# Kernel tuning notes

Hardware: AMD Instinct MI355X
Metric: run time of the kernel (lower is better)

The kernel has to match this reference:

```python
import jax, jax.numpy as jnp
import numpy as np

N_NODES = 100000


def gcn_conv(x, W, src, dst, n):
    """PyG GCNConv with bias=False: add self-loops, symmetric norm, scatter-add."""
    h = x @ W  # [N, out]
    # degree including self-loop (all edge weights = 1)
    deg = jnp.zeros((n,), dtype=x.dtype).at[dst].add(1.0) + 1.0
    inv_sqrt = jax.lax.rsqrt(deg)  # deg >= 1 so safe
    edge_norm = inv_sqrt[src] * inv_sqrt[dst]  # [E]
    # neighbor aggregation: out_i = sum_{j->i} norm_ji * h_j
    agg = jnp.zeros_like(h).at[dst].add(h[src] * edge_norm[:, None])
    # self-loop contribution: norm_ii = 1/deg_i
    return agg + h * (inv_sqrt * inv_sqrt)[:, None]


def setup_inputs() -> dict:
    key = jax.random.key(0)
    k1, k2, k3, k4 = jax.random.split(key, 4)
    x = jax.random.normal(k1, (N_NODES, 128), dtype=jnp.float32)
    edge_index = jax.random.randint(k2, (2, 1600000), 0, N_NODES, dtype=jnp.int32)
    W1 = jax.random.normal(k3, (128, 64), dtype=jnp.float32) * (1.0 / np.sqrt(128))
    W2 = jax.random.normal(k4, (64, 40), dtype=jnp.float32) * (1.0 / np.sqrt(64))
    return {"x": x, "edge_index": edge_index, "W1": W1, "W2": W2}


def reference(x, edge_index, W1, W2):
    n = x.shape[0]
    src, dst = edge_index[0], edge_index[1]
    # layer 1 (dropout p=0.0 is identity) + relu
    h = jax.nn.relu(gcn_conv(x, W1, src, dst, n))
    # layer 2 + relu, then squeeze
    out = jax.nn.relu(gcn_conv(h, W2, src, dst, n))
    return jnp.squeeze(out)
```

## Files before the change

kernel.cpp:

```cpp
#include <hip/hip_runtime.h>
#include <hip/hip_fp16.h>


#define F0 128
#define F1 64
#define F2 40
#define SCAN_B 512
#define GEMM_BLKS 768
#define NRANK (GEMM_BLKS / 3)

__global__ void k_zero(int* __restrict__ cnt, int n) {
    const int i = blockIdx.x * blockDim.x + threadIdx.x;
    if (i < n) cnt[i] = 0;
}

__global__ __launch_bounds__(256) void k_gemmrank(const float* __restrict__ x,
                                                  const float* __restrict__ W,
                                                  __half* __restrict__ h,
                                                  const int* __restrict__ ei,
                                                  int* __restrict__ cnt,
                                                  int* __restrict__ rank,
                                                  int n, int E) {
    __shared__ float Wl[F0 * F1];
    __shared__ float xs[32 * F0];
    const int bid = blockIdx.x;
    const int tid = threadIdx.x;

    if ((bid % 3) == 2) {
        const int rb = bid / 3;
        const int stride = NRANK * 256;
#pragma unroll 4
        for (int e = rb * 256 + tid; e < E; e += stride)
            rank[e] = atomicAdd(&cnt[ei[E + e]], 1);
        return;
    }

    const int gid = bid - bid / 3;
    const int c = tid & 63;
    const int rq = tid >> 6;

    {
        float4* Wl4 = (float4*)Wl;
        const float4* Wg4 = (const float4*)W;
#pragma unroll
        for (int j = 0; j < (F0 * F1 / 4) / 256; ++j)
            Wl4[j * 256 + tid] = Wg4[j * 256 + tid];
    }
    __syncthreads();

    const int NG = GEMM_BLKS - NRANK;
    const int ntiles = (n + 31) >> 5;
    for (int tile = gid; tile < ntiles; tile += NG) {
        float4* xs4w = (float4*)xs;
#pragma unroll
        for (int j = 0; j < 4; ++j) {
            int fi = j * 256 + tid;
            int row = fi >> 5;
            int rg = tile * 32 + row;
            if (rg > n - 1) rg = n - 1;
            const float4* xrow = (const float4*)(x + (long long)rg * F0);
            xs4w[fi] = xrow[fi & 31];
        }
        __syncthreads();

        float acc[8] = {0.f,0.f,0.f,0.f,0.f,0.f,0.f,0.f};
#pragma unroll 2
        for (int b = 0; b < 32; ++b) {
            const float w0 = Wl[(4 * b + 0) * F1 + c];
            const float w1 = Wl[(4 * b + 1) * F1 + c];
            const float w2 = Wl[(4 * b + 2) * F1 + c];
            const float w3 = Wl[(4 * b + 3) * F1 + c];
#pragma unroll
            for (int i = 0; i < 8; ++i) {
                float4 xv = ((const float4*)xs)[(rq * 8 + i) * 32 + b];
                acc[i] = fmaf(xv.w, w3, fmaf(xv.z, w2, fmaf(xv.y, w1, fmaf(xv.x, w0, acc[i]))));
            }
        }

#pragma unroll
        for (int i = 0; i < 8; ++i) {
            int rg = tile * 32 + rq * 8 + i;
            if (rg < n) h[(long long)rg * F1 + c] = __float2half(acc[i]);
        }
        __syncthreads();
    }
}

__global__ __launch_bounds__(SCAN_B) void k_rsqrt_bsum(const int* __restrict__ cnt,
                                                       float* __restrict__ invs,
                                                       int* __restrict__ bsum, int n) {
    __shared__ int s[SCAN_B];
    const int t = threadIdx.x;
    const int i = blockIdx.x * SCAN_B + t;
    int c = 0;
    if (i < n) {
        c = cnt[i];
        invs[i] = rsqrtf((float)(c + 1));
    }
    s[t] = c;
    __syncthreads();
    for (int off = SCAN_B / 2; off > 0; off >>= 1) {
        if (t < off) s[t] += s[t + off];
        __syncthreads();
    }
    if (t == 0) bsum[blockIdx.x] = s[0];
}

__global__ __launch_bounds__(1024) void k_bscan(int* __restrict__ bsum, int nb) {
    __shared__ int s[1024];
    const int t = threadIdx.x;
    const int orig = (t < nb) ? bsum[t] : 0;
    s[t] = orig;
    __syncthreads();
    for (int off = 1; off < 1024; off <<= 1) {
        int add = (t >= off) ? s[t - off] : 0;
        __syncthreads();
        s[t] += add;
        __syncthreads();
    }
    if (t < nb) bsum[t] = s[t] - orig;
}

__global__ __launch_bounds__(SCAN_B) void k_scan3(const int* __restrict__ cnt,
                                                  const int* __restrict__ bsum,
                                                  int* __restrict__ rowptr, int n) {
    __shared__ int s[SCAN_B];
    const int t = threadIdx.x;
    const int i = blockIdx.x * SCAN_B + t;
    const int orig = (i < n) ? cnt[i] : 0;
    s[t] = orig;
    __syncthreads();
    for (int off = 1; off < SCAN_B; off <<= 1) {
        int add = (t >= off) ? s[t - off] : 0;
        __syncthreads();
        s[t] += add;
        __syncthreads();
    }
    const int excl = s[t] - orig + bsum[blockIdx.x];
    if (i < n) rowptr[i] = excl;
    if (i == n - 1) rowptr[n] = excl + orig;
}

__global__ void k_fill_scale(const int* __restrict__ ei, const int* __restrict__ rank,
                             const int* __restrict__ rowptr, int* __restrict__ csr4,
                             __half* __restrict__ h, const float* __restrict__ invs,
                             int E, int n, int gFILL) {
    const int bid = blockIdx.x;
    const int tid = threadIdx.x;
    if (bid < gFILL) {
        int e = bid * 1024 + tid;
#pragma unroll
        for (int j = 0; j < 4; ++j, e += 256) {
            if (e < E) {
                const int s = ei[e];
                const int d = ei[E + e];
                csr4[rowptr[d] + rank[e]] = s;
            }
        }
    } else {
        const int fb = bid - gFILL;
        const long long total4 = (long long)n * F1 / 4;
        long long i4 = (long long)fb * 256 + tid;
        const long long stride = (long long)2048 * 256;
        for (; i4 < total4; i4 += stride) {
            const int r = (int)(i4 >> 4);
            const float iv = invs[r];
            __half2* hp = (__half2*)h + i4 * 2;
            __half2 a = hp[0], b = hp[1];
            float2 af = __half22float2(a), bf = __half22float2(b);
            af.x *= iv; af.y *= iv; bf.x *= iv; bf.y *= iv;
            hp[0] = __float22half2_rn(af);
            hp[1] = __float22half2_rn(bf);
        }
    }
}

__global__ __launch_bounds__(256) void k_gemm2(const float* __restrict__ x,
                                               const float* __restrict__ W,
                                               const float* __restrict__ invs,
                                               __half* __restrict__ h, int n) {
    __shared__ float Wl[F1 * F2];
    __shared__ float xs[32 * F1];
    const int tid = threadIdx.x;
    const int c = tid & 63;
    const int rq = tid >> 6;

    for (int i = tid; i < F1 * F2; i += 256) Wl[i] = W[i];
    __syncthreads();

    const int ntiles = (n + 31) >> 5;
    for (int tile = blockIdx.x; tile < ntiles; tile += gridDim.x) {
        float4* xs4w = (float4*)xs;
#pragma unroll
        for (int j = 0; j < 2; ++j) {
            int fi = j * 256 + tid;
            int row = fi >> 4;
            int rg = tile * 32 + row;
            if (rg > n - 1) rg = n - 1;
            const float4* xrow = (const float4*)(x + (long long)rg * F1);
            xs4w[fi] = xrow[fi & 15];
        }
        __syncthreads();

        if (c < F2) {
            float acc[8] = {0.f,0.f,0.f,0.f,0.f,0.f,0.f,0.f};
#pragma unroll 2
            for (int b = 0; b < 16; ++b) {
                const float w0 = Wl[(4 * b + 0) * F2 + c];
                const float w1 = Wl[(4 * b + 1) * F2 + c];
                const float w2 = Wl[(4 * b + 2) * F2 + c];
                const float w3 = Wl[(4 * b + 3) * F2 + c];
#pragma unroll
                for (int i = 0; i < 8; ++i) {
                    float4 xv = ((const float4*)xs)[(rq * 8 + i) * 16 + b];
                    acc[i] = fmaf(xv.w, w3, fmaf(xv.z, w2, fmaf(xv.y, w1, fmaf(xv.x, w0, acc[i]))));
                }
            }
#pragma unroll
            for (int i = 0; i < 8; ++i) {
                int rg = tile * 32 + rq * 8 + i;
                if (rg < n) h[(long long)rg * F2 + c] = __float2half(acc[i] * invs[rg]);
            }
        }
        __syncthreads();
    }
}

__global__ __launch_bounds__(256) void k_gather64(const int* __restrict__ rowptr,
                                                  const int* __restrict__ csr4,
                                                  const float* __restrict__ invs,
                                                  const __half* __restrict__ h,
                                                  float* __restrict__ g, int n) {
    const int w = (blockIdx.x * blockDim.x + threadIdx.x) >> 6;
    const int lane = threadIdx.x & 63;
    if (w >= n) return;
    const int beg = rowptr[w];
    const int end = rowptr[w + 1];
    float acc0 = 0.f, acc1 = 0.f, acc2 = 0.f, acc3 = 0.f;
    int k = beg;
    for (; k + 8 <= end; k += 8) {
        const int s0 = csr4[k+0], s1 = csr4[k+1], s2 = csr4[k+2], s3 = csr4[k+3];
        const int s4 = csr4[k+4], s5 = csr4[k+5], s6 = csr4[k+6], s7 = csr4[k+7];
        const float v0 = __half2float(h[(long long)s0 * F1 + lane]);
        const float v1 = __half2float(h[(long long)s1 * F1 + lane]);
        const float v2 = __half2float(h[(long long)s2 * F1 + lane]);
        const float v3 = __half2float(h[(long long)s3 * F1 + lane]);
        const float v4 = __half2float(h[(long long)s4 * F1 + lane]);
        const float v5 = __half2float(h[(long long)s5 * F1 + lane]);
        const float v6 = __half2float(h[(long long)s6 * F1 + lane]);
        const float v7 = __half2float(h[(long long)s7 * F1 + lane]);
        acc0 += v0 + v4; acc1 += v1 + v5; acc2 += v2 + v6; acc3 += v3 + v7;
    }
    for (; k + 2 <= end; k += 2) {
        const int s0 = csr4[k], s1 = csr4[k+1];
        acc0 += __half2float(h[(long long)s0 * F1 + lane]);
        acc1 += __half2float(h[(long long)s1 * F1 + lane]);
    }
    if (k < end) {
        const int s0 = csr4[k];
        acc0 += __half2float(h[(long long)s0 * F1 + lane]);
    }
    const float iv = invs[w];
    const float self = __half2float(h[(long long)w * F1 + lane]);
    g[(long long)w * F1 + lane] = fmaxf(iv * (((acc0 + acc1) + (acc2 + acc3)) + self), 0.f);
}

__global__ __launch_bounds__(256) void k_gather40(const int* __restrict__ rowptr,
                                                  const int* __restrict__ csr4,
                                                  const float* __restrict__ invs,
                                                  const __half* __restrict__ h,
                                                  float* __restrict__ g, int n) {
    const int w = (blockIdx.x * blockDim.x + threadIdx.x) >> 6;
    const int lane = threadIdx.x & 63;
    if (w >= n) return;
    const int beg = rowptr[w];
    const int end = rowptr[w + 1];
    float acc0 = 0.f, acc1 = 0.f, acc2 = 0.f, acc3 = 0.f;
    int k = beg;
    if (lane < F2) {
        for (; k + 8 <= end; k += 8) {
            const int s0 = csr4[k+0], s1 = csr4[k+1], s2 = csr4[k+2], s3 = csr4[k+3];
            const int s4 = csr4[k+4], s5 = csr4[k+5], s6 = csr4[k+6], s7 = csr4[k+7];
            const float v0 = __half2float(h[(long long)s0 * F2 + lane]);
            const float v1 = __half2float(h[(long long)s1 * F2 + lane]);
            const float v2 = __half2float(h[(long long)s2 * F2 + lane]);
            const float v3 = __half2float(h[(long long)s3 * F2 + lane]);
            const float v4 = __half2float(h[(long long)s4 * F2 + lane]);
            const float v5 = __half2float(h[(long long)s5 * F2 + lane]);
            const float v6 = __half2float(h[(long long)s6 * F2 + lane]);
            const float v7 = __half2float(h[(long long)s7 * F2 + lane]);
            acc0 += v0 + v4; acc1 += v1 + v5; acc2 += v2 + v6; acc3 += v3 + v7;
        }
        for (; k + 2 <= end; k += 2) {
            const int s0 = csr4[k], s1 = csr4[k+1];
            acc0 += __half2float(h[(long long)s0 * F2 + lane]);
            acc1 += __half2float(h[(long long)s1 * F2 + lane]);
        }
        if (k < end) {
            const int s0 = csr4[k];
            acc0 += __half2float(h[(long long)s0 * F2 + lane]);
        }
        const float iv = invs[w];
        const float self = __half2float(h[(long long)w * F2 + lane]);
        g[(long long)w * F2 + lane] = fmaxf(iv * (((acc0 + acc1) + (acc2 + acc3)) + self), 0.f);
    }
}

extern "C" void kernel_launch(void* const* d_in, const int* in_sizes, int n_in,
                              void* d_out, int out_size, void* d_ws, size_t ws_size,
                              hipStream_t stream) {
    const float* x  = (const float*)d_in[0];
    const int*   ei = (const int*)d_in[1];
    const float* W1 = (const float*)d_in[2];
    const float* W2 = (const float*)d_in[3];
    float* out = (float*)d_out;
    const int n = in_sizes[0] / F0;
    const int E = in_sizes[1] / 2;

    const size_t np = ((size_t)n + 65) & ~(size_t)63;
    char* wsb = (char*)d_ws;
    int*    cnt    = (int*)wsb;
    int*    rowptr = cnt + np;
    float*  invs   = (float*)(rowptr + np);
    int*    rank   = (int*)(invs + np);
    int*    csr4   = rank + E;
    __half* h1h    = (__half*)(csr4 + E);
    float*  g1     = (float*)(h1h + (size_t)n * F1);
    int*    bsum   = (int*)(g1 + (size_t)n * F1);
    __half* h2h    = h1h;

    const int nb = (n + SCAN_B - 1) / SCAN_B;
    const int gN = (n + 255) / 256;
    const int gW = (int)(((long long)n * 64 + 255) / 256);
    const int gFILL = (E + 1023) / 1024;
    const int gFS = gFILL + 2048;

    hipLaunchKernelGGL(k_zero,      dim3(gN), dim3(256), 0, stream, cnt, n);
    hipLaunchKernelGGL(k_gemmrank,  dim3(GEMM_BLKS), dim3(256), 0, stream,
                       x, W1, h1h, ei, cnt, rank, n, E);
    hipLaunchKernelGGL(k_rsqrt_bsum, dim3(nb), dim3(SCAN_B), 0, stream, cnt, invs, bsum, n);
    hipLaunchKernelGGL(k_bscan,      dim3(1),  dim3(1024), 0, stream, bsum, nb);
    hipLaunchKernelGGL(k_scan3,      dim3(nb), dim3(SCAN_B), 0, stream, cnt, bsum, rowptr, n);
    hipLaunchKernelGGL(k_fill_scale, dim3(gFS), dim3(256), 0, stream,
                       ei, rank, rowptr, csr4, h1h, invs, E, n, gFILL);

    hipLaunchKernelGGL(k_gather64, dim3(gW), dim3(256), 0, stream, rowptr, csr4, invs, h1h, g1, n);
    hipLaunchKernelGGL(k_gemm2,    dim3(GEMM_BLKS), dim3(256), 0, stream, g1, W2, invs, h2h, n);
    hipLaunchKernelGGL(k_gather40, dim3(gW), dim3(256), 0, stream, rowptr, csr4, invs, h2h, out, n);
}
```

Baseline: 249.3 us.

## Split node range in halves and overlap fill, gather64 and gemm2 across stages

The CSR fill is split by destination-node half: the first half is filled alongside the h1 scaling, then a fused stage kernel fills the second half while gathering layer 1 for the first half. A second stage runs gemm2 on the first half while gathering the second half, and a final gemm2 covers the remaining half. h2 gets its own buffer instead of aliasing h1. The goal is to overlap independent work inside fused launches and keep the GPU busier, at the cost of each fill block reading the edge list twice and an extra launch.

```diff
diff --git a/kernel.cpp b/kernel.cpp
--- a/kernel.cpp
+++ b/kernel.cpp
@@ -8,6 +8,7 @@
 #define SCAN_B 512
 #define GEMM_BLKS 768
 #define NRANK (GEMM_BLKS / 3)
+#define STG_GM 512
 
 __global__ void k_zero(int* __restrict__ cnt, int n) {
     const int i = blockIdx.x * blockDim.x + threadIdx.x;
@@ -141,55 +142,42 @@
     if (i == n - 1) rowptr[n] = excl + orig;
 }
 
-__global__ void k_fill_scale(const int* __restrict__ ei, const int* __restrict__ rank,
-                             const int* __restrict__ rowptr, int* __restrict__ csr4,
-                             __half* __restrict__ h, const float* __restrict__ invs,
-                             int E, int n, int gFILL) {
-    const int bid = blockIdx.x;
-    const int tid = threadIdx.x;
-    if (bid < gFILL) {
-        int e = bid * 1024 + tid;
-#pragma unroll
-        for (int j = 0; j < 4; ++j, e += 256) {
-            if (e < E) {
-                const int s = ei[e];
-                const int d = ei[E + e];
-                csr4[rowptr[d] + rank[e]] = s;
-            }
-        }
-    } else {
-        const int fb = bid - gFILL;
-        const long long total4 = (long long)n * F1 / 4;
-        long long i4 = (long long)fb * 256 + tid;
-        const long long stride = (long long)2048 * 256;
-        for (; i4 < total4; i4 += stride) {
-            const int r = (int)(i4 >> 4);
-            const float iv = invs[r];
-            __half2* hp = (__half2*)h + i4 * 2;
-            __half2 a = hp[0], b = hp[1];
-            float2 af = __half22float2(a), bf = __half22float2(b);
-            af.x *= iv; af.y *= iv; bf.x *= iv; bf.y *= iv;
-            hp[0] = __float22half2_rn(af);
-            hp[1] = __float22half2_rn(bf);
-        }
-    }
-}
-
-__global__ __launch_bounds__(256) void k_gemm2(const float* __restrict__ x,
-                                               const float* __restrict__ W,
-                                               const float* __restrict__ invs,
-                                               __half* __restrict__ h, int n) {
+
+__device__ __forceinline__ void fill_body(const int* __restrict__ ei,
+                                          const int* __restrict__ rank,
+                                          const int* __restrict__ rowptr,
+                                          int* __restrict__ csr4,
+                                          int E, int flo, int fhi, int relbid,
+                                          int tid) {
+    int e = relbid * 1024 + tid;
+#pragma unroll
+    for (int j = 0; j < 4; ++j, e += 256) {
+        if (e < E) {
+            const int d = ei[E + e];
+            if (d >= flo && d < fhi)
+                csr4[rowptr[d] + rank[e]] = ei[e];
+        }
+    }
+}
+
+__device__ __forceinline__ void gemm2_body(const float* __restrict__ g,
+                                           const float* __restrict__ W,
+                                           const float* __restrict__ invs,
+                                           __half* __restrict__ h,
+                                           int n, int lo, int hi,
+                                           int relbid, int nblk, int tid) {
     __shared__ float Wl[F1 * F2];
     __shared__ float xs[32 * F1];
-    const int tid = threadIdx.x;
     const int c = tid & 63;
     const int rq = tid >> 6;
 
     for (int i = tid; i < F1 * F2; i += 256) Wl[i] = W[i];
     __syncthreads();
 
-    const int ntiles = (n + 31) >> 5;
-    for (int tile = blockIdx.x; tile < ntiles; tile += gridDim.x) {
+    const int t0 = lo >> 5;
+    const int ntiles = (hi - lo + 31) >> 5;
+    for (int ti = relbid; ti < ntiles; ti += nblk) {
+        const int tile = t0 + ti;
         float4* xs4w = (float4*)xs;
 #pragma unroll
         for (int j = 0; j < 2; ++j) {
@@ -197,7 +185,7 @@
             int row = fi >> 4;
             int rg = tile * 32 + row;
             if (rg > n - 1) rg = n - 1;
-            const float4* xrow = (const float4*)(x + (long long)rg * F1);
+            const float4* xrow = (const float4*)(g + (long long)rg * F1);
             xs4w[fi] = xrow[fi & 15];
         }
         __syncthreads();
@@ -219,21 +207,22 @@
 #pragma unroll
             for (int i = 0; i < 8; ++i) {
                 int rg = tile * 32 + rq * 8 + i;
-                if (rg < n) h[(long long)rg * F2 + c] = __float2half(acc[i] * invs[rg]);
+                if (rg < hi) h[(long long)rg * F2 + c] = __float2half(acc[i] * invs[rg]);
             }
         }
         __syncthreads();
     }
 }
 
-__global__ __launch_bounds__(256) void k_gather64(const int* __restrict__ rowptr,
-                                                  const int* __restrict__ csr4,
-                                                  const float* __restrict__ invs,
-                                                  const __half* __restrict__ h,
-                                                  float* __restrict__ g, int n) {
-    const int w = (blockIdx.x * blockDim.x + threadIdx.x) >> 6;
-    const int lane = threadIdx.x & 63;
-    if (w >= n) return;
+__device__ __forceinline__ void gather64_body(const int* __restrict__ rowptr,
+                                              const int* __restrict__ csr4,
+                                              const float* __restrict__ invs,
+                                              const __half* __restrict__ h,
+                                              float* __restrict__ g,
+                                              int lo, int hi, int relbid, int tid) {
+    const int w = lo + relbid * 4 + (tid >> 6);
+    const int lane = tid & 63;
+    if (w >= hi) return;
     const int beg = rowptr[w];
     const int end = rowptr[w + 1];
     float acc0 = 0.f, acc1 = 0.f, acc2 = 0.f, acc3 = 0.f;
@@ -257,12 +246,72 @@
         acc1 += __half2float(h[(long long)s1 * F1 + lane]);
     }
     if (k < end) {
-        const int s0 = csr4[k];
-        acc0 += __half2float(h[(long long)s0 * F1 + lane]);
+        acc0 += __half2float(h[(long long)csr4[k] * F1 + lane]);
     }
     const float iv = invs[w];
     const float self = __half2float(h[(long long)w * F1 + lane]);
     g[(long long)w * F1 + lane] = fmaxf(iv * (((acc0 + acc1) + (acc2 + acc3)) + self), 0.f);
+}
+
+
+__global__ void k_fill_scale(const int* __restrict__ ei, const int* __restrict__ rank,
+                             const int* __restrict__ rowptr, int* __restrict__ csr4,
+                             __half* __restrict__ h, const float* __restrict__ invs,
+                             int E, int n, int flo, int fhi, int gFILL) {
+    const int bid = blockIdx.x;
+    const int tid = threadIdx.x;
+    if (bid < gFILL) {
+        fill_body(ei, rank, rowptr, csr4, E, flo, fhi, bid, tid);
+    } else {
+        const int fb = bid - gFILL;
+        const long long total4 = (long long)n * F1 / 4;
+        long long i4 = (long long)fb * 256 + tid;
+        const long long stride = (long long)2048 * 256;
+        for (; i4 < total4; i4 += stride) {
+            const int r = (int)(i4 >> 4);
+            const float iv = invs[r];
+            __half2* hp = (__half2*)h + i4 * 2;
+            __half2 a = hp[0], b = hp[1];
+            float2 af = __half22float2(a), bf = __half22float2(b);
+            af.x *= iv; af.y *= iv; bf.x *= iv; bf.y *= iv;
+            hp[0] = __float22half2_rn(af);
+            hp[1] = __float22half2_rn(bf);
+        }
+    }
+}
+
+__global__ __launch_bounds__(256, 8) void k_stage(const float* __restrict__ g1,
+                                                  const float* __restrict__ W2,
+                                                  const float* __restrict__ invs,
+                                                  __half* __restrict__ h2,
+                                                  const int* __restrict__ ei,
+                                                  const int* __restrict__ rank,
+                                                  const int* __restrict__ rowptr,
+                                                  int* __restrict__ csr4,
+                                                  const __half* __restrict__ h1,
+                                                  float* __restrict__ g1out,
+                                                  int n, int E,
+                                                  int nGm, int gmlo, int gmhi,
+                                                  int nFill, int flo, int fhi,
+                                                  int g64lo, int g64hi) {
+    const int bid = blockIdx.x;
+    const int tid = threadIdx.x;
+    if (bid < nGm) {
+        gemm2_body(g1, W2, invs, h2, n, gmlo, gmhi, bid, nGm, tid);
+    } else if (bid < nGm + nFill) {
+        fill_body(ei, rank, rowptr, csr4, E, flo, fhi, bid - nGm, tid);
+    } else {
+        gather64_body(rowptr, csr4, invs, h1, g1out, g64lo, g64hi,
+                      bid - nGm - nFill, tid);
+    }
+}
+
+__global__ __launch_bounds__(256) void k_gemm2(const float* __restrict__ g,
+                                               const float* __restrict__ W,
+                                               const float* __restrict__ invs,
+                                               __half* __restrict__ h,
+                                               int n, int lo, int hi) {
+    gemm2_body(g, W, invs, h, n, lo, hi, blockIdx.x, gridDim.x, threadIdx.x);
 }
 
 __global__ __launch_bounds__(256) void k_gather40(const int* __restrict__ rowptr,
@@ -297,8 +346,7 @@
             acc1 += __half2float(h[(long long)s1 * F2 + lane]);
         }
         if (k < end) {
-            const int s0 = csr4[k];
-            acc0 += __half2float(h[(long long)s0 * F2 + lane]);
+            acc0 += __half2float(h[(long long)csr4[k] * F2 + lane]);
         }
         const float iv = invs[w];
         const float self = __half2float(h[(long long)w * F2 + lane]);
@@ -326,14 +374,16 @@
     int*    csr4   = rank + E;
     __half* h1h    = (__half*)(csr4 + E);
     float*  g1     = (float*)(h1h + (size_t)n * F1);
-    int*    bsum   = (int*)(g1 + (size_t)n * F1);
-    __half* h2h    = h1h;
-
+    __half* h2h    = (__half*)(g1 + (size_t)n * F1);
+    int*    bsum   = (int*)(h2h + (size_t)n * F2);
+
+    const int nh = ((n / 2 + 31) / 32) * 32;
     const int nb = (n + SCAN_B - 1) / SCAN_B;
     const int gN = (n + 255) / 256;
+    const int gFILL = (E + 1023) / 1024;
+    const int nA = (nh + 3) / 4;
+    const int nB = (n - nh + 3) / 4;
     const int gW = (int)(((long long)n * 64 + 255) / 256);
-    const int gFILL = (E + 1023) / 1024;
-    const int gFS = gFILL + 2048;
 
     hipLaunchKernelGGL(k_zero,      dim3(gN), dim3(256), 0, stream, cnt, n);
     hipLaunchKernelGGL(k_gemmrank,  dim3(GEMM_BLKS), dim3(256), 0, stream,
@@ -341,10 +391,17 @@
     hipLaunchKernelGGL(k_rsqrt_bsum, dim3(nb), dim3(SCAN_B), 0, stream, cnt, invs, bsum, n);
     hipLaunchKernelGGL(k_bscan,      dim3(1),  dim3(1024), 0, stream, bsum, nb);
     hipLaunchKernelGGL(k_scan3,      dim3(nb), dim3(SCAN_B), 0, stream, cnt, bsum, rowptr, n);
-    hipLaunchKernelGGL(k_fill_scale, dim3(gFS), dim3(256), 0, stream,
-                       ei, rank, rowptr, csr4, h1h, invs, E, n, gFILL);
-
-    hipLaunchKernelGGL(k_gather64, dim3(gW), dim3(256), 0, stream, rowptr, csr4, invs, h1h, g1, n);
-    hipLaunchKernelGGL(k_gemm2,    dim3(GEMM_BLKS), dim3(256), 0, stream, g1, W2, invs, h2h, n);
-    hipLaunchKernelGGL(k_gather40, dim3(gW), dim3(256), 0, stream, rowptr, csr4, invs, h2h, out, n);
-}
+
+    hipLaunchKernelGGL(k_fill_scale, dim3(gFILL + 2048), dim3(256), 0, stream,
+                       ei, rank, rowptr, csr4, h1h, invs, E, n, 0, nh, gFILL);
+    hipLaunchKernelGGL(k_stage, dim3(gFILL + nA), dim3(256), 0, stream,
+                       g1, W2, invs, h2h, ei, rank, rowptr, csr4, h1h, g1,
+                       n, E, 0, 0, 0, gFILL, nh, n, 0, nh);
+    hipLaunchKernelGGL(k_stage, dim3(STG_GM + nB), dim3(256), 0, stream,
+                       g1, W2, invs, h2h, ei, rank, rowptr, csr4, h1h, g1,
+                       n, E, STG_GM, 0, nh, 0, 0, 0, nh, n);
+    hipLaunchKernelGGL(k_gemm2, dim3(GEMM_BLKS), dim3(256), 0, stream,
+                       g1, W2, invs, h2h, n, nh, n);
+    hipLaunchKernelGGL(k_gather40, dim3(gW), dim3(256), 0, stream,
+                       rowptr, csr4, invs, h2h, out, n);
+}
```

Result: no change. 252.4 us (+1.3%).
